# Kernel tuning notes

Hardware: AMD Instinct MI355X
Metric: run time of the kernel (lower is better)

## Reference

```python
import jax, jax.numpy as jnp
import numpy as np

N = 50000    # nodes in the (single, batch_size=1) graph
E = 800000   # edges
IN = 32      # in_dim per node
D1 = 16      # gcn_dim1
D2 = 16      # gcn_dim2
B = 8        # sample batch
EPS = 1e-5   # BatchNorm eps


def setup_inputs() -> dict:
    key = jax.random.key(0)
    ks = jax.random.split(key, 12)
    x = jax.random.normal(ks[0], (B, IN * N), dtype=jnp.float32)
    src = jax.random.randint(ks[1], (E,), 0, N)
    dst = jax.random.randint(ks[2], (E,), 0, N)
    W1 = jax.random.normal(ks[3], (IN, D1), dtype=jnp.float32) * 0.1
    b1 = jax.random.normal(ks[4], (D1,), dtype=jnp.float32) * 0.01
    g1_gamma = 1.0 + 0.1 * jax.random.normal(ks[5], (D1,), dtype=jnp.float32)
    g1_beta = 0.1 * jax.random.normal(ks[6], (D1,), dtype=jnp.float32)
    W2 = jax.random.normal(ks[7], (D1, D2), dtype=jnp.float32) * 0.1
    b2 = jax.random.normal(ks[8], (D2,), dtype=jnp.float32) * 0.01
    g2_gamma = 1.0 + 0.1 * jax.random.normal(ks[9], (D2,), dtype=jnp.float32)
    g2_beta = 0.1 * jax.random.normal(ks[10], (D2,), dtype=jnp.float32)
    n1_gamma = 1.0 + 0.1 * jax.random.normal(ks[11], (D2,), dtype=jnp.float32)
    n1_beta = jnp.zeros((D2,), dtype=jnp.float32)
    return {"x": x, "W1": W1, "b1": b1, "g1_gamma": g1_gamma, "g1_beta": g1_beta,
            "W2": W2, "b2": b2, "g2_gamma": g2_gamma, "g2_beta": g2_beta,
            "n1_gamma": n1_gamma, "n1_beta": n1_beta, "src": src, "dst": dst}


def reference(x, W1, b1, g1_gamma, g1_beta, W2, b2, g2_gamma, g2_beta,
              n1_gamma, n1_beta, src, dst):
    # DGL GraphConv norm='both': degrees clamped to min 1
    ones = jnp.ones((src.shape[0],), jnp.float32)
    out_norm = jnp.clip(jax.ops.segment_sum(ones, src, num_segments=N), 1.0) ** -0.5  # [N]
    in_norm = jnp.clip(jax.ops.segment_sum(ones, dst, num_segments=N), 1.0) ** -0.5   # [N]

    def conv(h, W, b):  # h: [N, d_in] -> [N, d_out]
        h = (h @ W) * out_norm[:, None]
        agg = jax.ops.segment_sum(h[src], dst, num_segments=N)
        return agg * in_norm[:, None] + b

    def bn(h, gamma, beta):  # training-mode BatchNorm over leading axis
        mu = h.mean(0, keepdims=True)
        var = h.var(0, keepdims=True)  # biased, as torch uses for normalization
        return (h - mu) * jax.lax.rsqrt(var + EPS) * gamma + beta

    def per_sample(xs):  # xs: [N, IN]
        h = jax.nn.relu(bn(conv(xs, W1, b1), g1_gamma, g1_beta))
        h = jax.nn.relu(bn(conv(h, W2, b2), g2_gamma, g2_beta))
        return h.mean(axis=0)  # mean_nodes with batch_size=1 -> [D2]

    xb = jnp.transpose(x.reshape(B, IN, N), (0, 2, 1))  # [B, N, IN]
    hg = jax.vmap(per_sample)(xb)                       # [B, D2]
    # norm1 BatchNorm over the sample batch; dropout is eval-mode identity
    return bn(hg, n1_gamma, n1_beta)
```

## Files before the change

### kernel.cpp

```cpp
#include <hip/hip_runtime.h>

#define NN 50000
#define NE 800000
#define IND 32
#define DD 16
#define BB 8
#define NC 128
#define EPSBN 1e-5f
#define SCB ((NN + 255) / 256)
#define G 128
#define CHE (NE / G)
#define WPN (NN / 4)

typedef unsigned int uint;
typedef unsigned short ushort;

__device__ __forceinline__ ushort f2bf(float f) {
  uint u = __float_as_uint(f);
  return (ushort)((u + 0x7fffu + ((u >> 16) & 1u)) >> 16);
}
__device__ __forceinline__ uint pack2bf(float lo, float hi) {
  return (uint)f2bf(lo) | ((uint)f2bf(hi) << 16);
}
__device__ __forceinline__ void add8(float* acc, uint4 v) {
  acc[0] += __uint_as_float(v.x << 16);
  acc[1] += __uint_as_float(v.x & 0xffff0000u);
  acc[2] += __uint_as_float(v.y << 16);
  acc[3] += __uint_as_float(v.y & 0xffff0000u);
  acc[4] += __uint_as_float(v.z << 16);
  acc[5] += __uint_as_float(v.z & 0xffff0000u);
  acc[6] += __uint_as_float(v.w << 16);
  acc[7] += __uint_as_float(v.w & 0xffff0000u);
}

__global__ __launch_bounds__(256) void k_hist(const int* __restrict__ src,
                                              const int* __restrict__ dst,
                                              uint* __restrict__ dstH,
                                              uint* __restrict__ srcH) {
  __shared__ uint h[WPN];
  int b = blockIdx.x;
  bool isDst = b < G;
  int cb = isDst ? b : b - G;
  const int* idx = isDst ? dst : src;
  uint* out = (isDst ? dstH : srcH) + (size_t)cb * WPN;
  for (int w = threadIdx.x; w < WPN; w += 256) h[w] = 0;
  __syncthreads();
  int base = cb * CHE;
  for (int k = threadIdx.x; k < CHE; k += 256) {
    int d = idx[base + k];
    atomicAdd(&h[d >> 2], 1u << ((d & 3) * 8));
  }
  __syncthreads();
  for (int w = threadIdx.x; w < WPN; w += 256) out[w] = h[w];
}

__global__ __launch_bounds__(256) void k_reduce(uint* __restrict__ dstH,
                                                const uint* __restrict__ srcH,
                                                int* __restrict__ degi,
                                                float* __restrict__ inorm,
                                                float* __restrict__ onorm) {
  int b = blockIdx.x;
  bool isDst = b < 49;
  int col = (isDst ? b : b - 49) * 256 + threadIdx.x;
  if (col >= WPN) return;
  if (isDst) {
    uint run = 0;
    for (int k = 0; k < G; k++) {
      size_t p = (size_t)k * WPN + col;
      uint v = dstH[p];
      dstH[p] = run;
      run += v;
    }
    int n0 = col * 4;
    int4 dv;
    float4 nv;
    int c0 = run & 255, c1 = (run >> 8) & 255, c2 = (run >> 16) & 255, c3 = (run >> 24) & 255;
    dv.x = c0; dv.y = c1; dv.z = c2; dv.w = c3;
    nv.x = rsqrtf((float)(c0 > 1 ? c0 : 1));
    nv.y = rsqrtf((float)(c1 > 1 ? c1 : 1));
    nv.z = rsqrtf((float)(c2 > 1 ? c2 : 1));
    nv.w = rsqrtf((float)(c3 > 1 ? c3 : 1));
    *(int4*)(degi + n0) = dv;
    *(float4*)(inorm + n0) = nv;
  } else {
    uint run = 0;
    for (int k = 0; k < G; k++) run += srcH[(size_t)k * WPN + col];
    int n0 = col * 4;
    float4 nv;
    int c0 = run & 255, c1 = (run >> 8) & 255, c2 = (run >> 16) & 255, c3 = (run >> 24) & 255;
    nv.x = rsqrtf((float)(c0 > 1 ? c0 : 1));
    nv.y = rsqrtf((float)(c1 > 1 ? c1 : 1));
    nv.z = rsqrtf((float)(c2 > 1 ? c2 : 1));
    nv.w = rsqrtf((float)(c3 > 1 ? c3 : 1));
    *(float4*)(onorm + n0) = nv;
  }
}

__global__ void k_scan1(const int* __restrict__ degi, int* __restrict__ bsum) {
  __shared__ int sh[256];
  int n = blockIdx.x * 256 + threadIdx.x;
  sh[threadIdx.x] = (n < NN) ? degi[n] : 0;
  __syncthreads();
  for (int o = 128; o > 0; o >>= 1) {
    if (threadIdx.x < o) sh[threadIdx.x] += sh[threadIdx.x + o];
    __syncthreads();
  }
  if (threadIdx.x == 0) bsum[blockIdx.x] = sh[0];
}

__global__ void k_scan2(const int* __restrict__ bsum, int* __restrict__ boff) {
  __shared__ int sh[256];
  int t = threadIdx.x;
  int v = (t < SCB) ? bsum[t] : 0;
  sh[t] = v;
  __syncthreads();
  for (int o = 1; o < 256; o <<= 1) {
    int u = (t >= o) ? sh[t - o] : 0;
    __syncthreads();
    sh[t] += u;
    __syncthreads();
  }
  if (t < SCB) boff[t] = sh[t] - v;
}

__global__ void k_scan3(const int* __restrict__ degi, const int* __restrict__ boff,
                        int* __restrict__ off) {
  __shared__ int sh[256];
  int n = blockIdx.x * 256 + threadIdx.x;
  int t = threadIdx.x;
  int v = (n < NN) ? degi[n] : 0;
  sh[t] = v;
  __syncthreads();
  for (int o = 1; o < 256; o <<= 1) {
    int u = (t >= o) ? sh[t - o] : 0;
    __syncthreads();
    sh[t] += u;
    __syncthreads();
  }
  if (n < NN) off[n] = boff[blockIdx.x] + sh[t] - v;
}

__global__ __launch_bounds__(512) void k_csr2(const int* __restrict__ src,
                                              const int* __restrict__ dst,
                                              const int* __restrict__ off,
                                              const uint* __restrict__ dstH,
                                              ushort* __restrict__ csr) {
  __shared__ uint cur[WPN];
  int b = blockIdx.x;
  for (int w = threadIdx.x; w < WPN; w += 512) cur[w] = 0;
  __syncthreads();
  const uint* bb = dstH + (size_t)b * WPN;
  int base = b * CHE;
  for (int k = threadIdx.x; k < CHE; k += 512) {
    int e = base + k;
    int d = dst[e];
    int sh = (d & 3) * 8;
    uint old = atomicAdd(&cur[d >> 2], 1u << sh);
    int rank = (old >> sh) & 255;
    int pre = (bb[d >> 2] >> sh) & 255;
    csr[off[d] + pre + rank] = (ushort)src[e];
  }
}

__global__ void k_gemm1(const float* __restrict__ x, const float* __restrict__ W1,
                        const float* __restrict__ onorm, ushort* __restrict__ Hb,
                        float* __restrict__ zeroRegion) {
  __shared__ float w[IND * DD];
  int tid = threadIdx.x;
  if (blockIdx.x == 0) {
    for (int i = tid; i < 5 * NC; i += 256) zeroRegion[i] = 0.f;
  }
  for (int i = tid; i < IND * DD; i += 256) w[i] = W1[i];
  __syncthreads();
  int gid = blockIdx.x * 256 + tid;
  if (gid >= BB * NN) return;
  int b = gid / NN;
  int n = gid - b * NN;
  const float* xb = x + (size_t)b * IND * NN + n;
  float acc[DD];
#pragma unroll
  for (int d = 0; d < DD; d++) acc[d] = 0.f;
  for (int i = 0; i < IND; i++) {
    float v = xb[(size_t)i * NN];
#pragma unroll
    for (int d = 0; d < DD; d++) acc[d] = fmaf(v, w[i * DD + d], acc[d]);
  }
  float on = onorm[n];
  uint p[8];
#pragma unroll
  for (int k = 0; k < 8; k++) p[k] = pack2bf(acc[2 * k] * on, acc[2 * k + 1] * on);
  uint* o4 = (uint*)(Hb + ((size_t)n * BB + b) * DD);
  *(uint4*)(o4) = make_uint4(p[0], p[1], p[2], p[3]);
  *(uint4*)(o4 + 4) = make_uint4(p[4], p[5], p[6], p[7]);
}

__global__ __launch_bounds__(256) void k_gather(const int* __restrict__ off,
                                                const int* __restrict__ degi,
                                                const ushort* __restrict__ csr,
                                                const ushort* __restrict__ Hb,
                                                float* __restrict__ AGG) {
  int gid = blockIdx.x * 256 + threadIdx.x;
  int n = gid >> 4;
  if (n >= NN) return;
  int q = (gid & 15) * 8;
  int o = off[n], dg = degi[n];
  const ushort* hq = Hb + q;
  float acc[8];
#pragma unroll
  for (int k = 0; k < 8; k++) acc[k] = 0.f;
  int j = 0;
  for (; j + 4 <= dg; j += 4) {
    int s0 = csr[o + j], s1 = csr[o + j + 1], s2 = csr[o + j + 2], s3 = csr[o + j + 3];
    uint4 v0 = *(const uint4*)(hq + (size_t)s0 * NC);
    uint4 v1 = *(const uint4*)(hq + (size_t)s1 * NC);
    uint4 v2 = *(const uint4*)(hq + (size_t)s2 * NC);
    uint4 v3 = *(const uint4*)(hq + (size_t)s3 * NC);
    add8(acc, v0);
    add8(acc, v1);
    add8(acc, v2);
    add8(acc, v3);
  }
  for (; j < dg; j++) {
    int s = csr[o + j];
    uint4 v = *(const uint4*)(hq + (size_t)s * NC);
    add8(acc, v);
  }
  float* op = AGG + (size_t)n * NC + q;
  *(float4*)(op) = make_float4(acc[0], acc[1], acc[2], acc[3]);
  *(float4*)(op + 4) = make_float4(acc[4], acc[5], acc[6], acc[7]);
}

__global__ void k_stats(const float* __restrict__ AGG, const float* __restrict__ inorm,
                        float* __restrict__ sum, float* __restrict__ sumsq) {
  __shared__ float sh[256];
  int c = threadIdx.x & (NC - 1);
  int r = threadIdx.x >> 7;
  float s = 0.f, ss = 0.f;
  for (int n = blockIdx.x * 2 + r; n < NN; n += gridDim.x * 2) {
    float a = AGG[(size_t)n * NC + c] * inorm[n];
    s += a;
    ss = fmaf(a, a, ss);
  }
  sh[threadIdx.x] = s;
  __syncthreads();
  if (r == 0) unsafeAtomicAdd(&sum[c], s + sh[threadIdx.x + 128]);
  __syncthreads();
  sh[threadIdx.x] = ss;
  __syncthreads();
  if (r == 0) unsafeAtomicAdd(&sumsq[c], ss + sh[threadIdx.x + 128]);
}

__global__ void k_applyg2(const float* __restrict__ AGG, const float* __restrict__ inorm,
                          const float* __restrict__ onorm, const float* __restrict__ sum,
                          const float* __restrict__ sumsq, const float* __restrict__ gamma,
                          const float* __restrict__ beta, const float* __restrict__ W2,
                          ushort* __restrict__ Hb) {
  __shared__ float w[DD * DD];
  __shared__ float ssc[NC], stc[NC];
  int tid = threadIdx.x;
  if (tid < DD * DD) w[tid] = W2[tid];
  if (tid < NC) {
    float mu = sum[tid] * (1.0f / NN);
    float var = fmaxf(sumsq[tid] * (1.0f / NN) - mu * mu, 0.f);
    int d = tid & (DD - 1);
    float s = gamma[d] * rsqrtf(var + EPSBN);
    ssc[tid] = s;
    stc[tid] = beta[d] - mu * s;
  }
  __syncthreads();
  int gid = blockIdx.x * 256 + tid;
  if (gid >= BB * NN) return;
  int n = gid >> 3, b = gid & 7;
  const float4* ap = (const float4*)(AGG + (size_t)gid * DD);
  float inn = inorm[n];
  float z[DD];
  float4 v0 = ap[0], v1 = ap[1], v2 = ap[2], v3 = ap[3];
  z[0] = v0.x; z[1] = v0.y; z[2] = v0.z; z[3] = v0.w;
  z[4] = v1.x; z[5] = v1.y; z[6] = v1.z; z[7] = v1.w;
  z[8] = v2.x; z[9] = v2.y; z[10] = v2.z; z[11] = v2.w;
  z[12] = v3.x; z[13] = v3.y; z[14] = v3.z; z[15] = v3.w;
#pragma unroll
  for (int d = 0; d < DD; d++) {
    int c = b * DD + d;
    z[d] = fmaxf(0.f, fmaf(z[d] * inn, ssc[c], stc[c]));
  }
  float on = onorm[n];
  float o[DD];
#pragma unroll
  for (int d2 = 0; d2 < DD; d2++) {
    float acc = 0.f;
#pragma unroll
    for (int d = 0; d < DD; d++) acc = fmaf(z[d], w[d * DD + d2], acc);
    o[d2] = acc * on;
  }
  uint p[8];
#pragma unroll
  for (int k = 0; k < 8; k++) p[k] = pack2bf(o[2 * k], o[2 * k + 1]);
  uint* op = (uint*)(Hb + (size_t)gid * DD);
  *(uint4*)(op) = make_uint4(p[0], p[1], p[2], p[3]);
  *(uint4*)(op + 4) = make_uint4(p[4], p[5], p[6], p[7]);
}

__global__ void k_final(const float* __restrict__ AGG, const float* __restrict__ inorm,
                        const float* __restrict__ sum, const float* __restrict__ sumsq,
                        const float* __restrict__ gamma, const float* __restrict__ beta,
                        float* __restrict__ hgsum) {
  __shared__ float sh[256];
  __shared__ float ssc[NC], stc[NC];
  int tid = threadIdx.x;
  if (tid < NC) {
    float mu = sum[tid] * (1.0f / NN);
    float var = fmaxf(sumsq[tid] * (1.0f / NN) - mu * mu, 0.f);
    int d = tid & (DD - 1);
    float s = gamma[d] * rsqrtf(var + EPSBN);
    ssc[tid] = s;
    stc[tid] = beta[d] - mu * s;
  }
  __syncthreads();
  int c = tid & (NC - 1);
  int r = tid >> 7;
  float scc = ssc[c], tcc = stc[c];
  float s = 0.f;
  for (int n = blockIdx.x * 2 + r; n < NN; n += gridDim.x * 2) {
    float a = AGG[(size_t)n * NC + c] * inorm[n];
    s += fmaxf(0.f, fmaf(a, scc, tcc));
  }
  sh[tid] = s;
  __syncthreads();
  if (r == 0) unsafeAtomicAdd(&hgsum[c], s + sh[tid + 128]);
}

__global__ void k_out(const float* __restrict__ hgsum, const float* __restrict__ g,
                      const float* __restrict__ bt, float* __restrict__ out) {
  __shared__ float sh[NC];
  int c = threadIdx.x;
  float hg = hgsum[c] * (1.0f / NN);
  sh[c] = hg;
  __syncthreads();
  int d = c & (DD - 1);
  float mu = 0.f;
#pragma unroll
  for (int b = 0; b < BB; b++) mu += sh[b * DD + d];
  mu *= (1.0f / BB);
  float var = 0.f;
#pragma unroll
  for (int b = 0; b < BB; b++) { float t = sh[b * DD + d] - mu; var = fmaf(t, t, var); }
  var *= (1.0f / BB);
  out[c] = fmaf((hg - mu) * rsqrtf(var + EPSBN), g[d], bt[d]);
}

extern "C" void kernel_launch(void* const* d_in, const int* in_sizes, int n_in,
                              void* d_out, int out_size, void* d_ws, size_t ws_size,
                              hipStream_t stream) {
  const float* x   = (const float*)d_in[0];
  const float* W1  = (const float*)d_in[1];
  const float* g1g = (const float*)d_in[3];
  const float* g1b = (const float*)d_in[4];
  const float* W2  = (const float*)d_in[5];
  const float* g2g = (const float*)d_in[7];
  const float* g2b = (const float*)d_in[8];
  const float* n1g = (const float*)d_in[9];
  const float* n1b = (const float*)d_in[10];
  const int* src   = (const int*)d_in[11];
  const int* dst   = (const int*)d_in[12];
  float* out = (float*)d_out;

  char* w = (char*)d_ws;
  float* AGG   = (float*)w; w += (size_t)NN * NC * 4;
  ushort* Hb   = (ushort*)w; w += (size_t)NN * NC * 2;
  int* degi    = (int*)w;   w += (size_t)NN * 4;
  int* off     = (int*)w;   w += (size_t)NN * 4;
  ushort* csr  = (ushort*)w; w += (size_t)NE * 2;
  float* onorm = (float*)w; w += (size_t)NN * 4;
  float* inorm = (float*)w; w += (size_t)NN * 4;
  int* bsum    = (int*)w;   w += (size_t)SCB * 4;
  int* boff    = (int*)w;   w += (size_t)SCB * 4;
  float* sum1  = (float*)w; w += NC * 4;
  float* sq1   = (float*)w; w += NC * 4;
  float* sum2  = (float*)w; w += NC * 4;
  float* sq2   = (float*)w; w += NC * 4;
  float* hgsum = (float*)w; w += NC * 4;

  uint* dstH = (uint*)AGG;
  uint* srcH = dstH + (size_t)G * WPN;

  k_hist<<<2 * G, 256, 0, stream>>>(src, dst, dstH, srcH);
  k_reduce<<<98, 256, 0, stream>>>(dstH, srcH, degi, inorm, onorm);
  k_scan1<<<SCB, 256, 0, stream>>>(degi, bsum);
  k_scan2<<<1, 256, 0, stream>>>(bsum, boff);
  k_scan3<<<SCB, 256, 0, stream>>>(degi, boff, off);
  k_csr2<<<G, 512, 0, stream>>>(src, dst, off, dstH, csr);
  k_gemm1<<<(BB * NN + 255) / 256, 256, 0, stream>>>(x, W1, onorm, Hb, sum1);
  k_gather<<<(NN * 16 + 255) / 256, 256, 0, stream>>>(off, degi, csr, Hb, AGG);
  k_stats<<<512, 256, 0, stream>>>(AGG, inorm, sum1, sq1);
  k_applyg2<<<(BB * NN + 255) / 256, 256, 0, stream>>>(AGG, inorm, onorm, sum1, sq1,
                                                       g1g, g1b, W2, Hb);
  k_gather<<<(NN * 16 + 255) / 256, 256, 0, stream>>>(off, degi, csr, Hb, AGG);
  k_stats<<<512, 256, 0, stream>>>(AGG, inorm, sum2, sq2);
  k_final<<<512, 256, 0, stream>>>(AGG, inorm, sum2, sq2, g2g, g2b, hgsum);
  k_out<<<1, NC, 0, stream>>>(hgsum, n1g, n1b, out);
}
```

Before: 230.6 us.

## Fuse BN stats into gather, merge scan kernels, restage gemm1 output via LDS

```diff
diff --git a/kernel.cpp b/kernel.cpp
--- a/kernel.cpp
+++ b/kernel.cpp
@@ -11,6 +11,8 @@
 #define G 128
 #define CHE (NE / G)
 #define WPN (NN / 4)
+#define GNB 125
+#define NGB 3125
 
 typedef unsigned int uint;
 typedef unsigned short ushort;
@@ -58,36 +60,48 @@
                                                 const uint* __restrict__ srcH,
                                                 int* __restrict__ degi,
                                                 float* __restrict__ inorm,
-                                                float* __restrict__ onorm) {
+                                                float* __restrict__ onorm,
+                                                int* __restrict__ bsum) {
+  __shared__ int sh[256];
   int b = blockIdx.x;
   bool isDst = b < 49;
-  int col = (isDst ? b : b - 49) * 256 + threadIdx.x;
-  if (col >= WPN) return;
+  int cb = isDst ? b : b - 49;
+  int col = cb * 256 + threadIdx.x;
+  bool valid = col < WPN;
   if (isDst) {
-    uint run = 0;
-    for (int k = 0; k < G; k++) {
-      size_t p = (size_t)k * WPN + col;
-      uint v = dstH[p];
-      dstH[p] = run;
-      run += v;
+    int degsum = 0;
+    if (valid) {
+      uint run = 0;
+      for (int k = 0; k < G; k++) {
+        size_t p = (size_t)k * WPN + col;
+        uint v = dstH[p];
+        dstH[p] = run;
+        run += v;
+      }
+      int n0 = col * 4;
+      int c0 = run & 255, c1 = (run >> 8) & 255, c2 = (run >> 16) & 255, c3 = (run >> 24) & 255;
+      degsum = c0 + c1 + c2 + c3;
+      *(int4*)(degi + n0) = make_int4(c0, c1, c2, c3);
+      float4 nv;
+      nv.x = rsqrtf((float)(c0 > 1 ? c0 : 1));
+      nv.y = rsqrtf((float)(c1 > 1 ? c1 : 1));
+      nv.z = rsqrtf((float)(c2 > 1 ? c2 : 1));
+      nv.w = rsqrtf((float)(c3 > 1 ? c3 : 1));
+      *(float4*)(inorm + n0) = nv;
     }
-    int n0 = col * 4;
-    int4 dv;
-    float4 nv;
-    int c0 = run & 255, c1 = (run >> 8) & 255, c2 = (run >> 16) & 255, c3 = (run >> 24) & 255;
-    dv.x = c0; dv.y = c1; dv.z = c2; dv.w = c3;
-    nv.x = rsqrtf((float)(c0 > 1 ? c0 : 1));
-    nv.y = rsqrtf((float)(c1 > 1 ? c1 : 1));
-    nv.z = rsqrtf((float)(c2 > 1 ? c2 : 1));
-    nv.w = rsqrtf((float)(c3 > 1 ? c3 : 1));
-    *(int4*)(degi + n0) = dv;
-    *(float4*)(inorm + n0) = nv;
-  } else {
+    sh[threadIdx.x] = degsum;
+    __syncthreads();
+    for (int o = 32; o > 0; o >>= 1) {
+      if ((threadIdx.x & 63) < o) sh[threadIdx.x] += sh[threadIdx.x + o];
+      __syncthreads();
+    }
+    if ((threadIdx.x & 63) == 0) bsum[b * 4 + (threadIdx.x >> 6)] = sh[threadIdx.x];
+  } else if (valid) {
     uint run = 0;
     for (int k = 0; k < G; k++) run += srcH[(size_t)k * WPN + col];
     int n0 = col * 4;
+    int c0 = run & 255, c1 = (run >> 8) & 255, c2 = (run >> 16) & 255, c3 = (run >> 24) & 255;
     float4 nv;
-    int c0 = run & 255, c1 = (run >> 8) & 255, c2 = (run >> 16) & 255, c3 = (run >> 24) & 255;
     nv.x = rsqrtf((float)(c0 > 1 ? c0 : 1));
     nv.y = rsqrtf((float)(c1 > 1 ? c1 : 1));
     nv.z = rsqrtf((float)(c2 > 1 ? c2 : 1));
@@ -96,22 +110,23 @@
   }
 }
 
-__global__ void k_scan1(const int* __restrict__ degi, int* __restrict__ bsum) {
+__global__ __launch_bounds__(256) void k_scan3(const int* __restrict__ degi,
+                                               const int* __restrict__ bsum,
+                                               int* __restrict__ off) {
   __shared__ int sh[256];
-  int n = blockIdx.x * 256 + threadIdx.x;
-  sh[threadIdx.x] = (n < NN) ? degi[n] : 0;
+  __shared__ int sboff;
+  int t = threadIdx.x;
+  int lim = blockIdx.x < SCB ? blockIdx.x : SCB;
+  sh[t] = (t < lim) ? bsum[t] : 0;
   __syncthreads();
   for (int o = 128; o > 0; o >>= 1) {
-    if (threadIdx.x < o) sh[threadIdx.x] += sh[threadIdx.x + o];
+    if (t < o) sh[t] += sh[t + o];
     __syncthreads();
   }
-  if (threadIdx.x == 0) bsum[blockIdx.x] = sh[0];
-}
-
-__global__ void k_scan2(const int* __restrict__ bsum, int* __restrict__ boff) {
-  __shared__ int sh[256];
-  int t = threadIdx.x;
-  int v = (t < SCB) ? bsum[t] : 0;
+  if (t == 0) sboff = sh[0];
+  __syncthreads();
+  int n = blockIdx.x * 256 + t;
+  int v = (n < NN) ? degi[n] : 0;
   sh[t] = v;
   __syncthreads();
   for (int o = 1; o < 256; o <<= 1) {
@@ -120,24 +135,7 @@
     sh[t] += u;
     __syncthreads();
   }
-  if (t < SCB) boff[t] = sh[t] - v;
-}
-
-__global__ void k_scan3(const int* __restrict__ degi, const int* __restrict__ boff,
-                        int* __restrict__ off) {
-  __shared__ int sh[256];
-  int n = blockIdx.x * 256 + threadIdx.x;
-  int t = threadIdx.x;
-  int v = (n < NN) ? degi[n] : 0;
-  sh[t] = v;
-  __syncthreads();
-  for (int o = 1; o < 256; o <<= 1) {
-    int u = (t >= o) ? sh[t - o] : 0;
-    __syncthreads();
-    sh[t] += u;
-    __syncthreads();
-  }
-  if (n < NN) off[n] = boff[blockIdx.x] + sh[t] - v;
+  if (n < NN) off[n] = sboff + sh[t] - v;
 }
 
 __global__ __launch_bounds__(512) void k_csr2(const int* __restrict__ src,
@@ -162,47 +160,60 @@
   }
 }
 
-__global__ void k_gemm1(const float* __restrict__ x, const float* __restrict__ W1,
-                        const float* __restrict__ onorm, ushort* __restrict__ Hb,
-                        float* __restrict__ zeroRegion) {
+__global__ __launch_bounds__(128) void k_gemm1(const float* __restrict__ x,
+                                               const float* __restrict__ W1,
+                                               const float* __restrict__ onorm,
+                                               ushort* __restrict__ Hb,
+                                               float* __restrict__ zeroRegion) {
   __shared__ float w[IND * DD];
+  __shared__ uint hb[GNB * 66];
   int tid = threadIdx.x;
   if (blockIdx.x == 0) {
-    for (int i = tid; i < 5 * NC; i += 256) zeroRegion[i] = 0.f;
-  }
-  for (int i = tid; i < IND * DD; i += 256) w[i] = W1[i];
-  __syncthreads();
-  int gid = blockIdx.x * 256 + tid;
-  if (gid >= BB * NN) return;
-  int b = gid / NN;
-  int n = gid - b * NN;
-  const float* xb = x + (size_t)b * IND * NN + n;
-  float acc[DD];
-#pragma unroll
-  for (int d = 0; d < DD; d++) acc[d] = 0.f;
-  for (int i = 0; i < IND; i++) {
-    float v = xb[(size_t)i * NN];
-#pragma unroll
-    for (int d = 0; d < DD; d++) acc[d] = fmaf(v, w[i * DD + d], acc[d]);
-  }
-  float on = onorm[n];
-  uint p[8];
-#pragma unroll
-  for (int k = 0; k < 8; k++) p[k] = pack2bf(acc[2 * k] * on, acc[2 * k + 1] * on);
-  uint* o4 = (uint*)(Hb + ((size_t)n * BB + b) * DD);
-  *(uint4*)(o4) = make_uint4(p[0], p[1], p[2], p[3]);
-  *(uint4*)(o4 + 4) = make_uint4(p[4], p[5], p[6], p[7]);
+    for (int i = tid; i < 5 * NC; i += 128) zeroRegion[i] = 0.f;
+  }
+  for (int i = tid; i < IND * DD; i += 128) w[i] = W1[i];
+  __syncthreads();
+  int n0 = blockIdx.x * GNB;
+  int n = n0 + tid;
+  if (tid < GNB) {
+    float on = onorm[n];
+    for (int b = 0; b < BB; b++) {
+      const float* xb = x + (size_t)b * IND * NN + n;
+      float acc[DD];
+#pragma unroll
+      for (int d = 0; d < DD; d++) acc[d] = 0.f;
+      for (int i = 0; i < IND; i++) {
+        float v = xb[(size_t)i * NN];
+#pragma unroll
+        for (int d = 0; d < DD; d++) acc[d] = fmaf(v, w[i * DD + d], acc[d]);
+      }
+#pragma unroll
+      for (int k = 0; k < 8; k++)
+        hb[tid * 66 + b * 8 + k] = pack2bf(acc[2 * k] * on, acc[2 * k + 1] * on);
+    }
+  }
+  __syncthreads();
+  uint4* outp = (uint4*)((uint*)Hb + (size_t)n0 * 64);
+  for (int g4 = tid; g4 < GNB * 16; g4 += 128) {
+    int nn = g4 >> 4, ww = (g4 & 15) * 4;
+    const uint* p = &hb[nn * 66 + ww];
+    outp[g4] = make_uint4(p[0], p[1], p[2], p[3]);
+  }
 }
 
 __global__ __launch_bounds__(256) void k_gather(const int* __restrict__ off,
                                                 const int* __restrict__ degi,
                                                 const ushort* __restrict__ csr,
                                                 const ushort* __restrict__ Hb,
-                                                float* __restrict__ AGG) {
-  int gid = blockIdx.x * 256 + threadIdx.x;
+                                                const float* __restrict__ inorm,
+                                                float* __restrict__ AGG,
+                                                float* __restrict__ psum,
+                                                float* __restrict__ psq) {
+  __shared__ float shs[2048], shq[2048];
+  int tid = threadIdx.x;
+  int gid = blockIdx.x * 256 + tid;
   int n = gid >> 4;
-  if (n >= NN) return;
-  int q = (gid & 15) * 8;
+  int q = (tid & 15) * 8;
   int o = off[n], dg = degi[n];
   const ushort* hq = Hb + q;
   float acc[8];
@@ -228,26 +239,45 @@
   float* op = AGG + (size_t)n * NC + q;
   *(float4*)(op) = make_float4(acc[0], acc[1], acc[2], acc[3]);
   *(float4*)(op + 4) = make_float4(acc[4], acc[5], acc[6], acc[7]);
-}
-
-__global__ void k_stats(const float* __restrict__ AGG, const float* __restrict__ inorm,
-                        float* __restrict__ sum, float* __restrict__ sumsq) {
+  float inn = inorm[n];
+#pragma unroll
+  for (int k = 0; k < 8; k++) {
+    float a = acc[k] * inn;
+    shs[tid * 8 + k] = a;
+    shq[tid * 8 + k] = a * a;
+  }
+  __syncthreads();
+  if (tid < 128) {
+    float s = 0.f, qq = 0.f;
+#pragma unroll
+    for (int slot = 0; slot < 16; slot++) {
+      s += shs[slot * 128 + tid];
+      qq += shq[slot * 128 + tid];
+    }
+    psum[blockIdx.x * 128 + tid] = s;
+    psq[blockIdx.x * 128 + tid] = qq;
+  }
+}
+
+__global__ __launch_bounds__(256) void k_statsr(const float* __restrict__ psum,
+                                                const float* __restrict__ psq,
+                                                float* __restrict__ sum,
+                                                float* __restrict__ sumsq) {
   __shared__ float sh[256];
-  int c = threadIdx.x & (NC - 1);
-  int r = threadIdx.x >> 7;
-  float s = 0.f, ss = 0.f;
-  for (int n = blockIdx.x * 2 + r; n < NN; n += gridDim.x * 2) {
-    float a = AGG[(size_t)n * NC + c] * inorm[n];
-    s += a;
-    ss = fmaf(a, a, ss);
-  }
-  sh[threadIdx.x] = s;
-  __syncthreads();
-  if (r == 0) unsafeAtomicAdd(&sum[c], s + sh[threadIdx.x + 128]);
-  __syncthreads();
-  sh[threadIdx.x] = ss;
-  __syncthreads();
-  if (r == 0) unsafeAtomicAdd(&sumsq[c], ss + sh[threadIdx.x + 128]);
+  int tid = threadIdx.x;
+  int c = tid & 127, h = tid >> 7;
+  float s = 0.f, q = 0.f;
+  for (int i = blockIdx.x * 2 + h; i < NGB; i += 128) {
+    s += psum[i * 128 + c];
+    q += psq[i * 128 + c];
+  }
+  sh[tid] = s;
+  __syncthreads();
+  if (h == 0) unsafeAtomicAdd(&sum[c], s + sh[tid + 128]);
+  __syncthreads();
+  sh[tid] = q;
+  __syncthreads();
+  if (h == 0) unsafeAtomicAdd(&sumsq[c], q + sh[tid + 128]);
 }
 
 __global__ void k_applyg2(const float* __restrict__ AGG, const float* __restrict__ inorm,
@@ -374,7 +404,8 @@
   float* onorm = (float*)w; w += (size_t)NN * 4;
   float* inorm = (float*)w; w += (size_t)NN * 4;
   int* bsum    = (int*)w;   w += (size_t)SCB * 4;
-  int* boff    = (int*)w;   w += (size_t)SCB * 4;
+  float* psum  = (float*)w; w += (size_t)NGB * NC * 4;
+  float* psq   = (float*)w; w += (size_t)NGB * NC * 4;
   float* sum1  = (float*)w; w += NC * 4;
   float* sq1   = (float*)w; w += NC * 4;
   float* sum2  = (float*)w; w += NC * 4;
@@ -385,18 +416,16 @@
   uint* srcH = dstH + (size_t)G * WPN;
 
   k_hist<<<2 * G, 256, 0, stream>>>(src, dst, dstH, srcH);
-  k_reduce<<<98, 256, 0, stream>>>(dstH, srcH, degi, inorm, onorm);
-  k_scan1<<<SCB, 256, 0, stream>>>(degi, bsum);
-  k_scan2<<<1, 256, 0, stream>>>(bsum, boff);
-  k_scan3<<<SCB, 256, 0, stream>>>(degi, boff, off);
+  k_reduce<<<98, 256, 0, stream>>>(dstH, srcH, degi, inorm, onorm, bsum);
+  k_scan3<<<SCB, 256, 0, stream>>>(degi, bsum, off);
   k_csr2<<<G, 512, 0, stream>>>(src, dst, off, dstH, csr);
-  k_gemm1<<<(BB * NN + 255) / 256, 256, 0, stream>>>(x, W1, onorm, Hb, sum1);
-  k_gather<<<(NN * 16 + 255) / 256, 256, 0, stream>>>(off, degi, csr, Hb, AGG);
-  k_stats<<<512, 256, 0, stream>>>(AGG, inorm, sum1, sq1);
+  k_gemm1<<<NN / GNB, 128, 0, stream>>>(x, W1, onorm, Hb, sum1);
+  k_gather<<<NGB, 256, 0, stream>>>(off, degi, csr, Hb, inorm, AGG, psum, psq);
+  k_statsr<<<64, 256, 0, stream>>>(psum, psq, sum1, sq1);
   k_applyg2<<<(BB * NN + 255) / 256, 256, 0, stream>>>(AGG, inorm, onorm, sum1, sq1,
                                                        g1g, g1b, W2, Hb);
-  k_gather<<<(NN * 16 + 255) / 256, 256, 0, stream>>>(off, degi, csr, Hb, AGG);
-  k_stats<<<512, 256, 0, stream>>>(AGG, inorm, sum2, sq2);
+  k_gather<<<NGB, 256, 0, stream>>>(off, degi, csr, Hb, inorm, AGG, psum, psq);
+  k_statsr<<<64, 256, 0, stream>>>(psum, psq, sum2, sq2);
   k_final<<<512, 256, 0, stream>>>(AGG, inorm, sum2, sq2, g2g, g2b, hgsum);
   k_out<<<1, NC, 0, stream>>>(hgsum, n1g, n1b, out);
 }
```

Measured after the change: 264.7 us. +14.8%, slower.
